# Kernel tuning notes

Measured on AMD Instinct MI355X. Metric: run time of the kernel, lower is better.

The kernel has to match this reference:

```python
import jax, jax.numpy as jnp
import numpy as np

N_NODES = 50000


def setup_inputs() -> dict:
    key = jax.random.key(0)
    ks = jax.random.split(key, 6)
    L, d = 3, 128
    x = jax.random.normal(ks[0], (N_NODES, d), dtype=jnp.float32)
    edge_index = jax.random.randint(ks[1], (2, 640000), 0, N_NODES, dtype=jnp.int64)
    s = 1.0 / np.sqrt(d)
    W1 = jax.random.normal(ks[2], (L, d, d), dtype=jnp.float32) * s
    W2 = jax.random.normal(ks[3], (L, d, d), dtype=jnp.float32) * s
    b1 = jnp.zeros((L, d), dtype=jnp.float32)
    b2 = jnp.zeros((L, d), dtype=jnp.float32)
    eps = jnp.zeros((L,), dtype=jnp.float32)
    final_w = jax.random.normal(ks[4], (d + L * d, d), dtype=jnp.float32) / np.sqrt(d + L * d)
    final_b = jnp.zeros((d,), dtype=jnp.float32)
    return {"x": x, "edge_index": edge_index, "W1": W1, "b1": b1,
            "W2": W2, "b2": b2, "eps": eps, "final_w": final_w, "final_b": final_b}


def reference(x, edge_index, W1, b1, W2, b2, eps, final_w, final_b):
    src, dst = edge_index[0], edge_index[1]
    num_layers = W1.shape[0]
    xs = [x]
    h = x
    for l in range(num_layers):
        # GINConv: sum-aggregate neighbor features, add (1+eps)*self, then 2-layer MLP
        agg = jax.ops.segment_sum(h[src], dst, num_segments=N_NODES)  # [N, d]
        z = (1.0 + eps[l]) * h + agg
        z = jax.nn.relu(z @ W1[l] + b1[l])
        h = jax.nn.relu(z @ W2[l] + b2[l])
        xs.append(h)
    out = jnp.concatenate(xs, axis=-1)  # [N, in + L*out]
    return out @ final_w + final_b
```

## Files before the change

### kernel.cpp

```cpp
#include <hip/hip_runtime.h>

#define NNODES 50000
#define NEDGES 640000
#define D 128

typedef unsigned short u16;
typedef unsigned int u32;
typedef __bf16 bf16x8 __attribute__((ext_vector_type(8)));
typedef float f32x4 __attribute__((ext_vector_type(4)));
union AB { uint4 u4; bf16x8 f; };

__device__ __forceinline__ u16 f2b(float f) {
    u32 u = __float_as_uint(f);
    return (u16)((u + 0x7fffu + ((u >> 16) & 1u)) >> 16);
}
__device__ __forceinline__ u32 pack2(float lo, float hi) {
    return (u32)f2b(lo) | ((u32)f2b(hi) << 16);
}
__device__ __forceinline__ float blo(u32 v) { return __uint_as_float(v << 16); }
__device__ __forceinline__ float bhi(u32 v) { return __uint_as_float(v & 0xffff0000u); }

__device__ __forceinline__ void acc8(float* a, uint4 v) {
    a[0] += blo(v.x); a[1] += bhi(v.x);
    a[2] += blo(v.y); a[3] += bhi(v.y);
    a[4] += blo(v.z); a[5] += bhi(v.z);
    a[6] += blo(v.w); a[7] += bhi(v.w);
}

__global__ void k_prep(const float* __restrict__ W1, const float* __restrict__ W2,
                       const float* __restrict__ fw, const float* __restrict__ x,
                       const int* __restrict__ dst,
                       u16* __restrict__ wT1, u16* __restrict__ wT2,
                       u16* __restrict__ fwTc, uint2* __restrict__ xb,
                       int* __restrict__ cnt, int* __restrict__ epos) {
    int idx = blockIdx.x * 256 + threadIdx.x;
    if (idx < 3 * 16384) {
        int l = idx >> 14, r = idx & 16383, n = r >> 7, k = r & 127;
        wT1[idx] = f2b(W1[l * 16384 + k * 128 + n]);
        wT2[idx] = f2b(W2[l * 16384 + k * 128 + n]);
    }
    if (idx < 4 * 16384) {
        int ch = idx >> 14, r = idx & 16383, n = r >> 7, k = r & 127;
        fwTc[idx] = f2b(fw[(ch * 128 + k) * 128 + n]);
    }
    if (idx < NEDGES) {
        epos[idx] = atomicAdd(&cnt[dst[idx]], 1);
    }
    if (idx < NNODES * 32) {
        float4 v = ((const float4*)x)[idx];
        xb[idx] = make_uint2(pack2(v.x, v.y), pack2(v.z, v.w));
    }
}

__global__ void k_scan1(const int* __restrict__ cnt, int* __restrict__ rp,
                        int* __restrict__ bsum, int* __restrict__ counter) {
    __shared__ int s[256];
    __shared__ int lastBlk;
    int tid = threadIdx.x;
    int i = blockIdx.x * 256 + tid;
    int v = (i < NNODES) ? cnt[i] : 0;
    s[tid] = v;
    __syncthreads();
    for (int off = 1; off < 256; off <<= 1) {
        int t = (tid >= off) ? s[tid - off] : 0;
        __syncthreads();
        s[tid] += t;
        __syncthreads();
    }
    if (i < NNODES) rp[i] = s[tid] - v;
    if (tid == 255)
        __hip_atomic_store(&bsum[blockIdx.x], s[255], __ATOMIC_RELEASE,
                           __HIP_MEMORY_SCOPE_AGENT);
    __syncthreads();
    if (tid == 0) {
        int n = __hip_atomic_fetch_add(counter, 1, __ATOMIC_ACQ_REL,
                                       __HIP_MEMORY_SCOPE_AGENT);
        lastBlk = (n == (int)gridDim.x - 1);
    }
    __syncthreads();
    if (lastBlk) {
        int nb = gridDim.x;
        int v2 = (tid < nb)
                     ? __hip_atomic_load(&bsum[tid], __ATOMIC_ACQUIRE,
                                         __HIP_MEMORY_SCOPE_AGENT)
                     : 0;
        s[tid] = v2;
        __syncthreads();
        for (int off = 1; off < 256; off <<= 1) {
            int t = (tid >= off) ? s[tid - off] : 0;
            __syncthreads();
            s[tid] += t;
            __syncthreads();
        }
        if (tid < nb) bsum[tid] = s[tid] - v2;
    }
}

__global__ void k_scatter(const int* __restrict__ src, const int* __restrict__ dst,
                          const int* __restrict__ rp, const int* __restrict__ bsum,
                          const int* __restrict__ epos, int* __restrict__ srcs) {
    int e = blockIdx.x * 256 + threadIdx.x;
    if (e < NEDGES) {
        int d = dst[e];
        srcs[rp[d] + bsum[d >> 8] + epos[e]] = src[e];
    }
}

__global__ void k_agg(const uint4* __restrict__ h4, const int* __restrict__ rp,
                      const int* __restrict__ bsum, const int* __restrict__ srcs,
                      const float* __restrict__ epsp, uint4* __restrict__ z4) {
    int tid = threadIdx.x;
    int c = tid & 15;
    int node = (blockIdx.x * 256 + tid) >> 4;
    int gbase = tid & 48;
    float sc = 1.0f + epsp[0];

    uint4 sv = h4[node * 16 + c];
    float acc[8];
    acc[0] = sc * blo(sv.x); acc[1] = sc * bhi(sv.x);
    acc[2] = sc * blo(sv.y); acc[3] = sc * bhi(sv.y);
    acc[4] = sc * blo(sv.z); acc[5] = sc * bhi(sv.z);
    acc[6] = sc * blo(sv.w); acc[7] = sc * bhi(sv.w);

    int beg = rp[node] + bsum[node >> 8];
    int end = (node + 1 == NNODES) ? NEDGES : rp[node + 1] + bsum[(node + 1) >> 8];
    for (int base = beg; base < end; base += 16) {
        int n = end - base; if (n > 16) n = 16;
        int myidx = (base + c < end) ? srcs[base + c] : 0;
        uint4 v[16];
#pragma unroll
        for (int j = 0; j < 16; ++j) {
            int s = __shfl(myidx, gbase + j, 64);
            v[j] = h4[s * 16 + c];
        }
#pragma unroll
        for (int j = 0; j < 16; ++j)
            if (j < n) acc8(acc, v[j]);
    }

    uint4 o;
    o.x = pack2(acc[0], acc[1]); o.y = pack2(acc[2], acc[3]);
    o.z = pack2(acc[4], acc[5]); o.w = pack2(acc[6], acc[7]);
    z4[node * 16 + c] = o;
}

template <bool FINAL>
__launch_bounds__(256, 2)
__global__ void k_mlp(const u16* __restrict__ A, const u16* __restrict__ wT1g,
                      const float* __restrict__ b1, const u16* __restrict__ wT2g,
                      const float* __restrict__ b2, u16* __restrict__ H,
                      const u16* __restrict__ xbg, const u16* __restrict__ h1g,
                      const u16* __restrict__ h2g, const u16* __restrict__ fwTc,
                      const float* __restrict__ fb, float* __restrict__ out) {
    __shared__ u16 Tb[128 * 128];
    __shared__ u16 wbuf[128 * 128];
    uint4* Tb4 = (uint4*)Tb;
    uint4* wb4 = (uint4*)wbuf;
    int tid = threadIdx.x;
    int r0 = blockIdx.x * 128;
    int wave = tid >> 6, lane = tid & 63, l16 = lane & 15, quad = lane >> 4;

    {
        const uint4* g = (const uint4*)wT1g;
        for (int i = tid; i < 2048; i += 256) {
            int n = i >> 4, ch = i & 15;
            wb4[n * 16 + ((ch + n) & 15)] = g[i];
        }
    }

    AB a[2][4];
#pragma unroll
    for (int s = 0; s < 2; ++s) {
        int row = r0 + wave * 32 + s * 16 + l16;
#pragma unroll
        for (int kb = 0; kb < 4; ++kb) {
            if (row < NNODES)
                a[s][kb].u4 = *(const uint4*)&A[row * 128 + kb * 32 + quad * 8];
            else
                a[s][kb].u4 = make_uint4(0, 0, 0, 0);
        }
    }
    __syncthreads();

    f32x4 acc[2][8];
#pragma unroll
    for (int col = 0; col < 8; ++col) {
        float bv = b1[col * 16 + l16];
        acc[0][col] = (f32x4){bv, bv, bv, bv};
        acc[1][col] = (f32x4){bv, bv, bv, bv};
    }
#pragma unroll
    for (int col = 0; col < 8; ++col) {
#pragma unroll
        for (int kb = 0; kb < 4; ++kb) {
            AB b;
            int n = col * 16 + l16;
            b.u4 = wb4[n * 16 + ((kb * 4 + quad + n) & 15)];
            acc[0][col] = __builtin_amdgcn_mfma_f32_16x16x32_bf16(a[0][kb].f, b.f, acc[0][col], 0, 0, 0);
            acc[1][col] = __builtin_amdgcn_mfma_f32_16x16x32_bf16(a[1][kb].f, b.f, acc[1][col], 0, 0, 0);
        }
    }

#pragma unroll
    for (int s = 0; s < 2; ++s)
#pragma unroll
        for (int col = 0; col < 8; ++col)
#pragma unroll
            for (int r = 0; r < 4; ++r) {
                int row = wave * 32 + s * 16 + quad * 4 + r;
                int kcol = col * 16 + l16;
                int ch = kcol >> 3;
                Tb[row * 128 + ((ch + row) & 15) * 8 + (kcol & 7)] =
                    f2b(fmaxf(acc[s][col][r], 0.f));
            }
    __syncthreads();

    {
        const uint4* g = (const uint4*)wT2g;
        for (int i = tid; i < 2048; i += 256) {
            int n = i >> 4, ch = i & 15;
            wb4[n * 16 + ((ch + n) & 15)] = g[i];
        }
    }
    AB a2[2][4];
#pragma unroll
    for (int s = 0; s < 2; ++s) {
        int m = wave * 32 + s * 16 + l16;
#pragma unroll
        for (int kb = 0; kb < 4; ++kb)
            a2[s][kb].u4 = Tb4[m * 16 + ((kb * 4 + quad + m) & 15)];
    }
    __syncthreads();

#pragma unroll
    for (int col = 0; col < 8; ++col) {
        float bv = b2[col * 16 + l16];
        acc[0][col] = (f32x4){bv, bv, bv, bv};
        acc[1][col] = (f32x4){bv, bv, bv, bv};
    }
#pragma unroll
    for (int col = 0; col < 8; ++col) {
#pragma unroll
        for (int kb = 0; kb < 4; ++kb) {
            AB b;
            int n = col * 16 + l16;
            b.u4 = wb4[n * 16 + ((kb * 4 + quad + n) & 15)];
            acc[0][col] = __builtin_amdgcn_mfma_f32_16x16x32_bf16(a2[0][kb].f, b.f, acc[0][col], 0, 0, 0);
            acc[1][col] = __builtin_amdgcn_mfma_f32_16x16x32_bf16(a2[1][kb].f, b.f, acc[1][col], 0, 0, 0);
        }
    }

#pragma unroll
    for (int s = 0; s < 2; ++s)
#pragma unroll
        for (int col = 0; col < 8; ++col)
#pragma unroll
            for (int r = 0; r < 4; ++r) {
                int row = wave * 32 + s * 16 + quad * 4 + r;
                int kcol = col * 16 + l16;
                int ch = kcol >> 3;
                Tb[row * 128 + ((ch + row) & 15) * 8 + (kcol & 7)] =
                    f2b(fmaxf(acc[s][col][r], 0.f));
            }

    if constexpr (!FINAL) {
        __syncthreads();
        for (int i = tid; i < 2048; i += 256) {
            int r = i >> 4, ch = i & 15;
            int grow = r0 + r;
            if (grow < NNODES)
                *(uint4*)&H[grow * 128 + ch * 8] = Tb4[r * 16 + ((ch + r) & 15)];
        }
    } else {
#pragma unroll
        for (int col = 0; col < 8; ++col) {
            float bv = fb[col * 16 + l16];
            acc[0][col] = (f32x4){bv, bv, bv, bv};
            acc[1][col] = (f32x4){bv, bv, bv, bv};
        }
        const u16* chin[3] = {xbg, h1g, h2g};
        AB afN[2][4];
#pragma unroll
        for (int s = 0; s < 2; ++s) {
            int row = r0 + wave * 32 + s * 16 + l16;
#pragma unroll
            for (int kb = 0; kb < 4; ++kb)
                afN[s][kb].u4 = (row < NNODES)
                                    ? *(const uint4*)&xbg[row * 128 + kb * 32 + quad * 8]
                                    : make_uint4(0, 0, 0, 0);
        }
#pragma unroll
        for (int chn = 0; chn < 4; ++chn) {
            __syncthreads();
            {
                const uint4* g = (const uint4*)(fwTc + chn * 16384);
                for (int i = tid; i < 2048; i += 256) {
                    int n = i >> 4, ch = i & 15;
                    wb4[n * 16 + ((ch + n) & 15)] = g[i];
                }
            }
            AB af[2][4];
#pragma unroll
            for (int s = 0; s < 2; ++s)
#pragma unroll
                for (int kb = 0; kb < 4; ++kb) af[s][kb] = afN[s][kb];
            if (chn < 2) {
                const u16* cp = chin[chn + 1];
#pragma unroll
                for (int s = 0; s < 2; ++s) {
                    int row = r0 + wave * 32 + s * 16 + l16;
#pragma unroll
                    for (int kb = 0; kb < 4; ++kb)
                        afN[s][kb].u4 = (row < NNODES)
                                            ? *(const uint4*)&cp[row * 128 + kb * 32 + quad * 8]
                                            : make_uint4(0, 0, 0, 0);
                }
            } else if (chn == 2) {
#pragma unroll
                for (int s = 0; s < 2; ++s) {
                    int m = wave * 32 + s * 16 + l16;
#pragma unroll
                    for (int kb = 0; kb < 4; ++kb)
                        afN[s][kb].u4 = Tb4[m * 16 + ((kb * 4 + quad + m) & 15)];
                }
            }
            __syncthreads();
#pragma unroll
            for (int col = 0; col < 8; ++col) {
#pragma unroll
                for (int kb = 0; kb < 4; ++kb) {
                    AB b;
                    int n = col * 16 + l16;
                    b.u4 = wb4[n * 16 + ((kb * 4 + quad + n) & 15)];
                    acc[0][col] = __builtin_amdgcn_mfma_f32_16x16x32_bf16(af[0][kb].f, b.f, acc[0][col], 0, 0, 0);
                    acc[1][col] = __builtin_amdgcn_mfma_f32_16x16x32_bf16(af[1][kb].f, b.f, acc[1][col], 0, 0, 0);
                }
            }
        }
#pragma unroll
        for (int s = 0; s < 2; ++s)
#pragma unroll
            for (int col = 0; col < 8; ++col)
#pragma unroll
                for (int r = 0; r < 4; ++r) {
                    int row = r0 + wave * 32 + s * 16 + quad * 4 + r;
                    if (row < NNODES)
                        __builtin_nontemporal_store(acc[s][col][r],
                                                    &out[row * 128 + col * 16 + l16]);
                }
    }
}

extern "C" void kernel_launch(void* const* d_in, const int* in_sizes, int n_in,
                              void* d_out, int out_size, void* d_ws, size_t ws_size,
                              hipStream_t stream) {
    const float* x   = (const float*)d_in[0];
    const int*   ei  = (const int*)d_in[1];
    const float* W1  = (const float*)d_in[2];
    const float* b1  = (const float*)d_in[3];
    const float* W2  = (const float*)d_in[4];
    const float* b2  = (const float*)d_in[5];
    const float* eps = (const float*)d_in[6];
    const float* fw  = (const float*)d_in[7];
    const float* fb  = (const float*)d_in[8];
    float* out = (float*)d_out;

    const int* srcA = ei;
    const int* dstA = ei + NEDGES;

    char* p = (char*)d_ws;
    size_t off = 0;
    auto take = [&](size_t bytes) {
        char* r = p + off;
        off = (off + bytes + 255) & ~(size_t)255;
        return r;
    };
    int* rp   = (int*)take((NNODES + 1) * sizeof(int));
    int* cnt  = (int*)take((NNODES + 1) * sizeof(int));
    int* bsum = (int*)take(256 * sizeof(int));
    int* epos = (int*)take(NEDGES * sizeof(int));
    int* srcs = (int*)take(NEDGES * sizeof(int));
    u16* wT1  = (u16*)take(3 * 16384 * sizeof(u16));
    u16* wT2  = (u16*)take(3 * 16384 * sizeof(u16));
    u16* fwTc = (u16*)take(4 * 16384 * sizeof(u16));
    u16* xb   = (u16*)take((size_t)NNODES * D * sizeof(u16));
    u16* zb   = (u16*)take((size_t)NNODES * D * sizeof(u16));
    u16* hb1  = (u16*)take((size_t)NNODES * D * sizeof(u16));
    u16* hb2  = (u16*)take((size_t)NNODES * D * sizeof(u16));
    (void)ws_size; (void)in_sizes; (void)n_in; (void)out_size;

    (void)hipMemsetAsync(cnt, 0, (NNODES + 1) * sizeof(int), stream);

    int nb = (NNODES + 255) / 256;
    k_prep<<<(NNODES * 32 + 255) / 256, 256, 0, stream>>>(W1, W2, fw, x, dstA,
                                                          wT1, wT2, fwTc, (uint2*)xb,
                                                          cnt, epos);
    k_scan1<<<nb, 256, 0, stream>>>(cnt, rp, bsum, cnt + NNODES);
    k_scatter<<<(NEDGES + 255) / 256, 256, 0, stream>>>(srcA, dstA, rp, bsum, epos, srcs);

    int gm = (NNODES + 127) / 128;
    k_agg<<<NNODES * 16 / 256, 256, 0, stream>>>((const uint4*)xb, rp, bsum, srcs, eps + 0, (uint4*)zb);
    k_mlp<false><<<gm, 256, 0, stream>>>(zb, wT1, b1, wT2, b2, hb1,
                                         nullptr, nullptr, nullptr, nullptr, nullptr, nullptr);
    k_agg<<<NNODES * 16 / 256, 256, 0, stream>>>((const uint4*)hb1, rp, bsum, srcs, eps + 1, (uint4*)zb);
    k_mlp<false><<<gm, 256, 0, stream>>>(zb, wT1 + 16384, b1 + D, wT2 + 16384, b2 + D, hb2,
                                         nullptr, nullptr, nullptr, nullptr, nullptr, nullptr);
    k_agg<<<NNODES * 16 / 256, 256, 0, stream>>>((const uint4*)hb2, rp, bsum, srcs, eps + 2, (uint4*)zb);
    k_mlp<true><<<gm, 256, 0, stream>>>(zb, wT1 + 2 * 16384, b1 + 2 * D,
                                        wT2 + 2 * 16384, b2 + 2 * D, nullptr,
                                        xb, hb1, hb2, fwTc, fb, out);
}
```

Before: 264.7 us.

## Split MLP kernel into 64-row tile variant for hidden layers; pack agg adds

Adds a dedicated k_mlp64 kernel for the two non-final GIN layers that processes 64 rows per block (one 16-row tile per wave) with smaller shared memory and launch bounds allowing 3 blocks per CU. The final layer keeps the 128-row tile kernel, now de-templated as k_mlpF. This aims to raise occupancy and the number of blocks so the MLP stages load-balance better across CUs. The trade-off is that each block loads the full weight matrices for half as many rows, doubling weight-staging traffic. The aggregation kernel also switches to float2 vector accumulators, which may let the compiler emit packed FP32 adds.

```diff
diff --git a/kernel.cpp b/kernel.cpp
--- a/kernel.cpp
+++ b/kernel.cpp
@@ -8,6 +8,7 @@
 typedef unsigned int u32;
 typedef __bf16 bf16x8 __attribute__((ext_vector_type(8)));
 typedef float f32x4 __attribute__((ext_vector_type(4)));
+typedef float f32x2 __attribute__((ext_vector_type(2)));
 union AB { uint4 u4; bf16x8 f; };
 
 __device__ __forceinline__ u16 f2b(float f) {
@@ -20,11 +21,11 @@
 __device__ __forceinline__ float blo(u32 v) { return __uint_as_float(v << 16); }
 __device__ __forceinline__ float bhi(u32 v) { return __uint_as_float(v & 0xffff0000u); }
 
-__device__ __forceinline__ void acc8(float* a, uint4 v) {
-    a[0] += blo(v.x); a[1] += bhi(v.x);
-    a[2] += blo(v.y); a[3] += bhi(v.y);
-    a[4] += blo(v.z); a[5] += bhi(v.z);
-    a[6] += blo(v.w); a[7] += bhi(v.w);
+__device__ __forceinline__ void acc8p(f32x2* a, uint4 v) {
+    a[0] += (f32x2){blo(v.x), bhi(v.x)};
+    a[1] += (f32x2){blo(v.y), bhi(v.y)};
+    a[2] += (f32x2){blo(v.z), bhi(v.z)};
+    a[3] += (f32x2){blo(v.w), bhi(v.w)};
 }
 
 __global__ void k_prep(const float* __restrict__ W1, const float* __restrict__ W2,
@@ -116,11 +117,11 @@
     float sc = 1.0f + epsp[0];
 
     uint4 sv = h4[node * 16 + c];
-    float acc[8];
-    acc[0] = sc * blo(sv.x); acc[1] = sc * bhi(sv.x);
-    acc[2] = sc * blo(sv.y); acc[3] = sc * bhi(sv.y);
-    acc[4] = sc * blo(sv.z); acc[5] = sc * bhi(sv.z);
-    acc[6] = sc * blo(sv.w); acc[7] = sc * bhi(sv.w);
+    f32x2 acc[4];
+    acc[0] = (f32x2){sc * blo(sv.x), sc * bhi(sv.x)};
+    acc[1] = (f32x2){sc * blo(sv.y), sc * bhi(sv.y)};
+    acc[2] = (f32x2){sc * blo(sv.z), sc * bhi(sv.z)};
+    acc[3] = (f32x2){sc * blo(sv.w), sc * bhi(sv.w)};
 
     int beg = rp[node] + bsum[node >> 8];
     int end = (node + 1 == NNODES) ? NEDGES : rp[node + 1] + bsum[(node + 1) >> 8];
@@ -135,23 +136,136 @@
         }
 #pragma unroll
         for (int j = 0; j < 16; ++j)
-            if (j < n) acc8(acc, v[j]);
+            if (j < n) acc8p(acc, v[j]);
     }
 
     uint4 o;
-    o.x = pack2(acc[0], acc[1]); o.y = pack2(acc[2], acc[3]);
-    o.z = pack2(acc[4], acc[5]); o.w = pack2(acc[6], acc[7]);
+    o.x = pack2(acc[0].x, acc[0].y); o.y = pack2(acc[1].x, acc[1].y);
+    o.z = pack2(acc[2].x, acc[2].y); o.w = pack2(acc[3].x, acc[3].y);
     z4[node * 16 + c] = o;
 }
 
-template <bool FINAL>
+__launch_bounds__(256, 3)
+__global__ void k_mlp64(const u16* __restrict__ A, const u16* __restrict__ wT1g,
+                        const float* __restrict__ b1, const u16* __restrict__ wT2g,
+                        const float* __restrict__ b2, u16* __restrict__ H) {
+    __shared__ u16 Tb[64 * 128];
+    __shared__ u16 wbuf[128 * 128];
+    uint4* Tb4 = (uint4*)Tb;
+    uint4* wb4 = (uint4*)wbuf;
+    int tid = threadIdx.x;
+    int r0 = blockIdx.x * 64;
+    int wave = tid >> 6, lane = tid & 63, l16 = lane & 15, quad = lane >> 4;
+
+    {
+        const uint4* g = (const uint4*)wT1g;
+        for (int i = tid; i < 2048; i += 256) {
+            int n = i >> 4, ch = i & 15;
+            wb4[n * 16 + ((ch + n) & 15)] = g[i];
+        }
+    }
+
+    AB a[4];
+    {
+        int row = r0 + wave * 16 + l16;
+#pragma unroll
+        for (int kb = 0; kb < 4; ++kb) {
+            if (row < NNODES)
+                a[kb].u4 = *(const uint4*)&A[row * 128 + kb * 32 + quad * 8];
+            else
+                a[kb].u4 = make_uint4(0, 0, 0, 0);
+        }
+    }
+    __syncthreads();
+
+    f32x4 acc[8];
+#pragma unroll
+    for (int col = 0; col < 8; ++col) {
+        float bv = b1[col * 16 + l16];
+        acc[col] = (f32x4){bv, bv, bv, bv};
+    }
+#pragma unroll
+    for (int col = 0; col < 8; ++col) {
+#pragma unroll
+        for (int kb = 0; kb < 4; ++kb) {
+            AB b;
+            int n = col * 16 + l16;
+            b.u4 = wb4[n * 16 + ((kb * 4 + quad + n) & 15)];
+            acc[col] = __builtin_amdgcn_mfma_f32_16x16x32_bf16(a[kb].f, b.f, acc[col], 0, 0, 0);
+        }
+    }
+
+#pragma unroll
+    for (int col = 0; col < 8; ++col)
+#pragma unroll
+        for (int r = 0; r < 4; ++r) {
+            int row = wave * 16 + quad * 4 + r;
+            int kcol = col * 16 + l16;
+            int ch = kcol >> 3;
+            Tb[row * 128 + ((ch + row) & 15) * 8 + (kcol & 7)] =
+                f2b(fmaxf(acc[col][r], 0.f));
+        }
+    __syncthreads();
+
+    {
+        const uint4* g = (const uint4*)wT2g;
+        for (int i = tid; i < 2048; i += 256) {
+            int n = i >> 4, ch = i & 15;
+            wb4[n * 16 + ((ch + n) & 15)] = g[i];
+        }
+    }
+    AB a2[4];
+    {
+        int m = wave * 16 + l16;
+#pragma unroll
+        for (int kb = 0; kb < 4; ++kb)
+            a2[kb].u4 = Tb4[m * 16 + ((kb * 4 + quad + m) & 15)];
+    }
+    __syncthreads();
+
+#pragma unroll
+    for (int col = 0; col < 8; ++col) {
+        float bv = b2[col * 16 + l16];
+        acc[col] = (f32x4){bv, bv, bv, bv};
+    }
+#pragma unroll
+    for (int col = 0; col < 8; ++col) {
+#pragma unroll
+        for (int kb = 0; kb < 4; ++kb) {
+            AB b;
+            int n = col * 16 + l16;
+            b.u4 = wb4[n * 16 + ((kb * 4 + quad + n) & 15)];
+            acc[col] = __builtin_amdgcn_mfma_f32_16x16x32_bf16(a2[kb].f, b.f, acc[col], 0, 0, 0);
+        }
+    }
+
+#pragma unroll
+    for (int col = 0; col < 8; ++col)
+#pragma unroll
+        for (int r = 0; r < 4; ++r) {
+            int row = wave * 16 + quad * 4 + r;
+            int kcol = col * 16 + l16;
+            int ch = kcol >> 3;
+            Tb[row * 128 + ((ch + row) & 15) * 8 + (kcol & 7)] =
+                f2b(fmaxf(acc[col][r], 0.f));
+        }
+    __syncthreads();
+
+    for (int i = tid; i < 1024; i += 256) {
+        int r = i >> 4, ch = i & 15;
+        int grow = r0 + r;
+        if (grow < NNODES)
+            *(uint4*)&H[grow * 128 + ch * 8] = Tb4[r * 16 + ((ch + r) & 15)];
+    }
+}
+
 __launch_bounds__(256, 2)
-__global__ void k_mlp(const u16* __restrict__ A, const u16* __restrict__ wT1g,
-                      const float* __restrict__ b1, const u16* __restrict__ wT2g,
-                      const float* __restrict__ b2, u16* __restrict__ H,
-                      const u16* __restrict__ xbg, const u16* __restrict__ h1g,
-                      const u16* __restrict__ h2g, const u16* __restrict__ fwTc,
-                      const float* __restrict__ fb, float* __restrict__ out) {
+__global__ void k_mlpF(const u16* __restrict__ A, const u16* __restrict__ wT1g,
+                       const float* __restrict__ b1, const u16* __restrict__ wT2g,
+                       const float* __restrict__ b2,
+                       const u16* __restrict__ xbg, const u16* __restrict__ h1g,
+                       const u16* __restrict__ h2g, const u16* __restrict__ fwTc,
+                       const float* __restrict__ fb, float* __restrict__ out) {
     __shared__ u16 Tb[128 * 128];
     __shared__ u16 wbuf[128 * 128];
     uint4* Tb4 = (uint4*)Tb;
@@ -263,92 +377,82 @@
                     f2b(fmaxf(acc[s][col][r], 0.f));
             }
 
-    if constexpr (!FINAL) {
+#pragma unroll
+    for (int col = 0; col < 8; ++col) {
+        float bv = fb[col * 16 + l16];
+        acc[0][col] = (f32x4){bv, bv, bv, bv};
+        acc[1][col] = (f32x4){bv, bv, bv, bv};
+    }
+    const u16* chin[3] = {xbg, h1g, h2g};
+    AB afN[2][4];
+#pragma unroll
+    for (int s = 0; s < 2; ++s) {
+        int row = r0 + wave * 32 + s * 16 + l16;
+#pragma unroll
+        for (int kb = 0; kb < 4; ++kb)
+            afN[s][kb].u4 = (row < NNODES)
+                                ? *(const uint4*)&xbg[row * 128 + kb * 32 + quad * 8]
+                                : make_uint4(0, 0, 0, 0);
+    }
+#pragma unroll
+    for (int chn = 0; chn < 4; ++chn) {
         __syncthreads();
-        for (int i = tid; i < 2048; i += 256) {
-            int r = i >> 4, ch = i & 15;
-            int grow = r0 + r;
-            if (grow < NNODES)
-                *(uint4*)&H[grow * 128 + ch * 8] = Tb4[r * 16 + ((ch + r) & 15)];
-        }
-    } else {
+        {
+            const uint4* g = (const uint4*)(fwTc + chn * 16384);
+            for (int i = tid; i < 2048; i += 256) {
+                int n = i >> 4, ch = i & 15;
+                wb4[n * 16 + ((ch + n) & 15)] = g[i];
+            }
+        }
+        AB af[2][4];
+#pragma unroll
+        for (int s = 0; s < 2; ++s)
+#pragma unroll
+            for (int kb = 0; kb < 4; ++kb) af[s][kb] = afN[s][kb];
+        if (chn < 2) {
+            const u16* cp = chin[chn + 1];
+#pragma unroll
+            for (int s = 0; s < 2; ++s) {
+                int row = r0 + wave * 32 + s * 16 + l16;
+#pragma unroll
+                for (int kb = 0; kb < 4; ++kb)
+                    afN[s][kb].u4 = (row < NNODES)
+                                        ? *(const uint4*)&cp[row * 128 + kb * 32 + quad * 8]
+                                        : make_uint4(0, 0, 0, 0);
+            }
+        } else if (chn == 2) {
+#pragma unroll
+            for (int s = 0; s < 2; ++s) {
+                int m = wave * 32 + s * 16 + l16;
+#pragma unroll
+                for (int kb = 0; kb < 4; ++kb)
+                    afN[s][kb].u4 = Tb4[m * 16 + ((kb * 4 + quad + m) & 15)];
+            }
+        }
+        __syncthreads();
 #pragma unroll
         for (int col = 0; col < 8; ++col) {
-            float bv = fb[col * 16 + l16];
-            acc[0][col] = (f32x4){bv, bv, bv, bv};
-            acc[1][col] = (f32x4){bv, bv, bv, bv};
-        }
-        const u16* chin[3] = {xbg, h1g, h2g};
-        AB afN[2][4];
-#pragma unroll
-        for (int s = 0; s < 2; ++s) {
-            int row = r0 + wave * 32 + s * 16 + l16;
-#pragma unroll
-            for (int kb = 0; kb < 4; ++kb)
-                afN[s][kb].u4 = (row < NNODES)
-                                    ? *(const uint4*)&xbg[row * 128 + kb * 32 + quad * 8]
-                                    : make_uint4(0, 0, 0, 0);
-        }
-#pragma unroll
-        for (int chn = 0; chn < 4; ++chn) {
-            __syncthreads();
-            {
-                const uint4* g = (const uint4*)(fwTc + chn * 16384);
-                for (int i = tid; i < 2048; i += 256) {
-                    int n = i >> 4, ch = i & 15;
-                    wb4[n * 16 + ((ch + n) & 15)] = g[i];
-                }
-            }
-            AB af[2][4];
-#pragma unroll
-            for (int s = 0; s < 2; ++s)
-#pragma unroll
-                for (int kb = 0; kb < 4; ++kb) af[s][kb] = afN[s][kb];
-            if (chn < 2) {
-                const u16* cp = chin[chn + 1];
-#pragma unroll
-                for (int s = 0; s < 2; ++s) {
-                    int row = r0 + wave * 32 + s * 16 + l16;
-#pragma unroll
-                    for (int kb = 0; kb < 4; ++kb)
-                        afN[s][kb].u4 = (row < NNODES)
-                                            ? *(const uint4*)&cp[row * 128 + kb * 32 + quad * 8]
-                                            : make_uint4(0, 0, 0, 0);
-                }
-            } else if (chn == 2) {
-#pragma unroll
-                for (int s = 0; s < 2; ++s) {
-                    int m = wave * 32 + s * 16 + l16;
-#pragma unroll
-                    for (int kb = 0; kb < 4; ++kb)
-                        afN[s][kb].u4 = Tb4[m * 16 + ((kb * 4 + quad + m) & 15)];
-                }
-            }
-            __syncthreads();
-#pragma unroll
-            for (int col = 0; col < 8; ++col) {
-#pragma unroll
-                for (int kb = 0; kb < 4; ++kb) {
-                    AB b;
-                    int n = col * 16 + l16;
-                    b.u4 = wb4[n * 16 + ((kb * 4 + quad + n) & 15)];
-                    acc[0][col] = __builtin_amdgcn_mfma_f32_16x16x32_bf16(af[0][kb].f, b.f, acc[0][col], 0, 0, 0);
-                    acc[1][col] = __builtin_amdgcn_mfma_f32_16x16x32_bf16(af[1][kb].f, b.f, acc[1][col], 0, 0, 0);
-                }
-            }
-        }
-#pragma unroll
-        for (int s = 0; s < 2; ++s)
-#pragma unroll
-            for (int col = 0; col < 8; ++col)
-#pragma unroll
-                for (int r = 0; r < 4; ++r) {
-                    int row = r0 + wave * 32 + s * 16 + quad * 4 + r;
-                    if (row < NNODES)
-                        __builtin_nontemporal_store(acc[s][col][r],
-                                                    &out[row * 128 + col * 16 + l16]);
-                }
-    }
+#pragma unroll
+            for (int kb = 0; kb < 4; ++kb) {
+                AB b;
+                int n = col * 16 + l16;
+                b.u4 = wb4[n * 16 + ((kb * 4 + quad + n) & 15)];
+                acc[0][col] = __builtin_amdgcn_mfma_f32_16x16x32_bf16(af[0][kb].f, b.f, acc[0][col], 0, 0, 0);
+                acc[1][col] = __builtin_amdgcn_mfma_f32_16x16x32_bf16(af[1][kb].f, b.f, acc[1][col], 0, 0, 0);
+            }
+        }
+    }
+#pragma unroll
+    for (int s = 0; s < 2; ++s)
+#pragma unroll
+        for (int col = 0; col < 8; ++col)
+#pragma unroll
+            for (int r = 0; r < 4; ++r) {
+                int row = r0 + wave * 32 + s * 16 + quad * 4 + r;
+                if (row < NNODES)
+                    __builtin_nontemporal_store(acc[s][col][r],
+                                                &out[row * 128 + col * 16 + l16]);
+            }
 }
 
 extern "C" void kernel_launch(void* const* d_in, const int* in_sizes, int n_in,
@@ -398,15 +502,13 @@
     k_scan1<<<nb, 256, 0, stream>>>(cnt, rp, bsum, cnt + NNODES);
     k_scatter<<<(NEDGES + 255) / 256, 256, 0, stream>>>(srcA, dstA, rp, bsum, epos, srcs);
 
-    int gm = (NNODES + 127) / 128;
+    int gm64 = (NNODES + 63) / 64;
     k_agg<<<NNODES * 16 / 256, 256, 0, stream>>>((const uint4*)xb, rp, bsum, srcs, eps + 0, (uint4*)zb);
-    k_mlp<false><<<gm, 256, 0, stream>>>(zb, wT1, b1, wT2, b2, hb1,
-                                         nullptr, nullptr, nullptr, nullptr, nullptr, nullptr);
+    k_mlp64<<<gm64, 256, 0, stream>>>(zb, wT1, b1, wT2, b2, hb1);
     k_agg<<<NNODES * 16 / 256, 256, 0, stream>>>((const uint4*)hb1, rp, bsum, srcs, eps + 1, (uint4*)zb);
-    k_mlp<false><<<gm, 256, 0, stream>>>(zb, wT1 + 16384, b1 + D, wT2 + 16384, b2 + D, hb2,
-                                         nullptr, nullptr, nullptr, nullptr, nullptr, nullptr);
+    k_mlp64<<<gm64, 256, 0, stream>>>(zb, wT1 + 16384, b1 + D, wT2 + 16384, b2 + D, hb2);
     k_agg<<<NNODES * 16 / 256, 256, 0, stream>>>((const uint4*)hb2, rp, bsum, srcs, eps + 2, (uint4*)zb);
-    k_mlp<true><<<gm, 256, 0, stream>>>(zb, wT1 + 2 * 16384, b1 + 2 * D,
-                                        wT2 + 2 * 16384, b2 + 2 * D, nullptr,
-                                        xb, hb1, hb2, fwTc, fb, out);
-}
+    k_mlpF<<<(NNODES + 127) / 128, 256, 0, stream>>>(zb, wT1 + 2 * 16384, b1 + 2 * D,
+                                                     wT2 + 2 * 16384, b2 + 2 * D,
+                                                     xb, hb1, hb2, fwTc, fb, out);
+}
```

Result: no change. 268.6 us (+1.5%).

## Read MLP weights directly from global memory instead of staging in LDS

Applied to the files above, without the earlier changes.

Removes the shared-memory weight buffer and reads B fragments for each MFMA straight from global/L2. This drops the weight staging loops and most __syncthreads, halves LDS use, and raises launch bounds to 4 blocks per SM for occupancy. The H writeback is remapped so each wave only touches rows it wrote, avoiding a barrier. The risk is repeated global weight loads per wave and higher latency on the MFMA operand path, plus register pressure under the tighter bound.

```diff
diff --git a/kernel.cpp b/kernel.cpp
--- a/kernel.cpp
+++ b/kernel.cpp
@@ -145,7 +145,7 @@
 }
 
 template <bool FINAL>
-__launch_bounds__(256, 2)
+__launch_bounds__(256, 4)
 __global__ void k_mlp(const u16* __restrict__ A, const u16* __restrict__ wT1g,
                       const float* __restrict__ b1, const u16* __restrict__ wT2g,
                       const float* __restrict__ b2, u16* __restrict__ H,
@@ -153,20 +153,10 @@
                       const u16* __restrict__ h2g, const u16* __restrict__ fwTc,
                       const float* __restrict__ fb, float* __restrict__ out) {
     __shared__ u16 Tb[128 * 128];
-    __shared__ u16 wbuf[128 * 128];
     uint4* Tb4 = (uint4*)Tb;
-    uint4* wb4 = (uint4*)wbuf;
     int tid = threadIdx.x;
     int r0 = blockIdx.x * 128;
     int wave = tid >> 6, lane = tid & 63, l16 = lane & 15, quad = lane >> 4;
-
-    {
-        const uint4* g = (const uint4*)wT1g;
-        for (int i = tid; i < 2048; i += 256) {
-            int n = i >> 4, ch = i & 15;
-            wb4[n * 16 + ((ch + n) & 15)] = g[i];
-        }
-    }
 
     AB a[2][4];
 #pragma unroll
@@ -180,7 +170,6 @@
                 a[s][kb].u4 = make_uint4(0, 0, 0, 0);
         }
     }
-    __syncthreads();
 
     f32x4 acc[2][8];
 #pragma unroll
@@ -194,8 +183,7 @@
 #pragma unroll
         for (int kb = 0; kb < 4; ++kb) {
             AB b;
-            int n = col * 16 + l16;
-            b.u4 = wb4[n * 16 + ((kb * 4 + quad + n) & 15)];
+            b.u4 = *(const uint4*)&wT1g[(col * 16 + l16) * 128 + kb * 32 + quad * 8];
             acc[0][col] = __builtin_amdgcn_mfma_f32_16x16x32_bf16(a[0][kb].f, b.f, acc[0][col], 0, 0, 0);
             acc[1][col] = __builtin_amdgcn_mfma_f32_16x16x32_bf16(a[1][kb].f, b.f, acc[1][col], 0, 0, 0);
         }
@@ -213,15 +201,7 @@
                 Tb[row * 128 + ((ch + row) & 15) * 8 + (kcol & 7)] =
                     f2b(fmaxf(acc[s][col][r], 0.f));
             }
-    __syncthreads();
-
-    {
-        const uint4* g = (const uint4*)wT2g;
-        for (int i = tid; i < 2048; i += 256) {
-            int n = i >> 4, ch = i & 15;
-            wb4[n * 16 + ((ch + n) & 15)] = g[i];
-        }
-    }
+
     AB a2[2][4];
 #pragma unroll
     for (int s = 0; s < 2; ++s) {
@@ -230,7 +210,6 @@
         for (int kb = 0; kb < 4; ++kb)
             a2[s][kb].u4 = Tb4[m * 16 + ((kb * 4 + quad + m) & 15)];
     }
-    __syncthreads();
 
 #pragma unroll
     for (int col = 0; col < 8; ++col) {
@@ -243,8 +222,7 @@
 #pragma unroll
         for (int kb = 0; kb < 4; ++kb) {
             AB b;
-            int n = col * 16 + l16;
-            b.u4 = wb4[n * 16 + ((kb * 4 + quad + n) & 15)];
+            b.u4 = *(const uint4*)&wT2g[(col * 16 + l16) * 128 + kb * 32 + quad * 8];
             acc[0][col] = __builtin_amdgcn_mfma_f32_16x16x32_bf16(a2[0][kb].f, b.f, acc[0][col], 0, 0, 0);
             acc[1][col] = __builtin_amdgcn_mfma_f32_16x16x32_bf16(a2[1][kb].f, b.f, acc[1][col], 0, 0, 0);
         }
@@ -264,9 +242,10 @@
             }
 
     if constexpr (!FINAL) {
-        __syncthreads();
-        for (int i = tid; i < 2048; i += 256) {
-            int r = i >> 4, ch = i & 15;
+#pragma unroll
+        for (int it = 0; it < 8; ++it) {
+            int r = wave * 32 + it * 4 + quad;
+            int ch = l16;
             int grow = r0 + r;
             if (grow < NNODES)
                 *(uint4*)&H[grow * 128 + ch * 8] = Tb4[r * 16 + ((ch + r) & 15)];
@@ -279,59 +258,36 @@
             acc[1][col] = (f32x4){bv, bv, bv, bv};
         }
         const u16* chin[3] = {xbg, h1g, h2g};
-        AB afN[2][4];
-#pragma unroll
-        for (int s = 0; s < 2; ++s) {
-            int row = r0 + wave * 32 + s * 16 + l16;
-#pragma unroll
-            for (int kb = 0; kb < 4; ++kb)
-                afN[s][kb].u4 = (row < NNODES)
-                                    ? *(const uint4*)&xbg[row * 128 + kb * 32 + quad * 8]
-                                    : make_uint4(0, 0, 0, 0);
-        }
 #pragma unroll
         for (int chn = 0; chn < 4; ++chn) {
-            __syncthreads();
-            {
-                const uint4* g = (const uint4*)(fwTc + chn * 16384);
-                for (int i = tid; i < 2048; i += 256) {
-                    int n = i >> 4, ch = i & 15;
-                    wb4[n * 16 + ((ch + n) & 15)] = g[i];
+            AB af[2][4];
+            if (chn < 3) {
+                const u16* cp = chin[chn];
+#pragma unroll
+                for (int s = 0; s < 2; ++s) {
+                    int row = r0 + wave * 32 + s * 16 + l16;
+#pragma unroll
+                    for (int kb = 0; kb < 4; ++kb)
+                        af[s][kb].u4 = (row < NNODES)
+                                           ? *(const uint4*)&cp[row * 128 + kb * 32 + quad * 8]
+                                           : make_uint4(0, 0, 0, 0);
+                }
+            } else {
+#pragma unroll
+                for (int s = 0; s < 2; ++s) {
+                    int m = wave * 32 + s * 16 + l16;
+#pragma unroll
+                    for (int kb = 0; kb < 4; ++kb)
+                        af[s][kb].u4 = Tb4[m * 16 + ((kb * 4 + quad + m) & 15)];
                 }
             }
-            AB af[2][4];
-#pragma unroll
-            for (int s = 0; s < 2; ++s)
-#pragma unroll
-                for (int kb = 0; kb < 4; ++kb) af[s][kb] = afN[s][kb];
-            if (chn < 2) {
-                const u16* cp = chin[chn + 1];
-#pragma unroll
-                for (int s = 0; s < 2; ++s) {
-                    int row = r0 + wave * 32 + s * 16 + l16;
-#pragma unroll
-                    for (int kb = 0; kb < 4; ++kb)
-                        afN[s][kb].u4 = (row < NNODES)
-                                            ? *(const uint4*)&cp[row * 128 + kb * 32 + quad * 8]
-                                            : make_uint4(0, 0, 0, 0);
-                }
-            } else if (chn == 2) {
-#pragma unroll
-                for (int s = 0; s < 2; ++s) {
-                    int m = wave * 32 + s * 16 + l16;
-#pragma unroll
-                    for (int kb = 0; kb < 4; ++kb)
-                        afN[s][kb].u4 = Tb4[m * 16 + ((kb * 4 + quad + m) & 15)];
-                }
-            }
-            __syncthreads();
+            const u16* fwc = fwTc + chn * 16384;
 #pragma unroll
             for (int col = 0; col < 8; ++col) {
 #pragma unroll
                 for (int kb = 0; kb < 4; ++kb) {
                     AB b;
-                    int n = col * 16 + l16;
-                    b.u4 = wb4[n * 16 + ((kb * 4 + quad + n) & 15)];
+                    b.u4 = *(const uint4*)&fwc[(col * 16 + l16) * 128 + kb * 32 + quad * 8];
                     acc[0][col] = __builtin_amdgcn_mfma_f32_16x16x32_bf16(af[0][kb].f, b.f, acc[0][col], 0, 0, 0);
                     acc[1][col] = __builtin_amdgcn_mfma_f32_16x16x32_bf16(af[1][kb].f, b.f, acc[1][col], 0, 0, 0);
                 }
```

Result: slower. 367.1 us (+38.7%).
